# Kernel optimization log

Hardware: AMD Instinct MI355X
Metric: run time of the kernel (lower is better)

## Reference

```python
import jax, jax.numpy as jnp
import numpy as np

B, S, D, H, HD, MLP = 2, 4096, 512, 8, 64, 2048
BLK, C = 128, 32  # Fixed1Pattern(block_size=128), Fixed2Pattern(block_size=128, c=32)
EPS = 1e-6


def _xavier(key, shape, fan_in, fan_out):
    lim = np.sqrt(6.0 / (fan_in + fan_out)).astype(np.float32)
    return jax.random.uniform(key, shape, jnp.float32, -lim, lim)


def setup_inputs() -> dict:
    key = jax.random.key(0)
    ks = jax.random.split(key, 9)
    return {
        "inputs": jax.random.normal(ks[0], (B, S, D), jnp.float32),
        "ln1_scale": jnp.ones((D,), jnp.float32),
        "ln1_bias": jnp.zeros((D,), jnp.float32),
        "wq": _xavier(ks[1], (D, H, HD), D, H * HD),
        "wk": _xavier(ks[2], (D, H, HD), D, H * HD),
        "wv": _xavier(ks[3], (D, H, HD), D, H * HD),
        "wo": _xavier(ks[4], (H, HD, D), H * HD, D),
        "ln2_scale": jnp.ones((D,), jnp.float32),
        "ln2_bias": jnp.zeros((D,), jnp.float32),
        "w1": _xavier(ks[5], (D, MLP), D, MLP),
        "b1": jax.random.normal(ks[6], (MLP,), jnp.float32) * 1e-6,
        "w2": _xavier(ks[7], (MLP, D), MLP, D),
        "b2": jax.random.normal(ks[8], (D,), jnp.float32) * 1e-6,
    }


def _layer_norm(x, scale, bias):
    mu = jnp.mean(x, axis=-1, keepdims=True)
    var = jnp.mean(jnp.square(x - mu), axis=-1, keepdims=True)
    return (x - mu) * jax.lax.rsqrt(var + EPS) * scale + bias


def _sparse_mask():
    # Union of causal Fixed1 (same block) and Fixed2 (last C columns of each block) patterns.
    i = jnp.arange(S)[:, None]
    j = jnp.arange(S)[None, :]
    causal = j <= i
    local = (i // BLK) == (j // BLK)            # Fixed1: within-block
    strided = (j % BLK) >= (BLK - C)            # Fixed2: block-summary columns
    return causal & (local | strided)           # [S, S] bool


def reference(inputs, ln1_scale, ln1_bias, wq, wk, wv, wo,
              ln2_scale, ln2_bias, w1, b1, w2, b2):
    x = _layer_norm(inputs, ln1_scale, ln1_bias)
    q = jnp.einsum("bsd,dhk->bshk", x, wq)
    k = jnp.einsum("bsd,dhk->bshk", x, wk)
    v = jnp.einsum("bsd,dhk->bshk", x, wv)
    scale = 1.0 / np.sqrt(HD).astype(np.float32)
    scores = jnp.einsum("bqhk,bshk->bhqs", q * scale, k)  # [B,H,S,S]
    mask = _sparse_mask()[None, None]
    scores = jnp.where(mask, scores, jnp.float32(-1e9))
    attn = jax.nn.softmax(scores, axis=-1)
    ctx = jnp.einsum("bhqs,bshk->bqhk", attn, v)
    attn_out = jnp.einsum("bqhk,hkd->bqd", ctx, wo)
    x = attn_out + inputs  # residual 1 (dropout deterministic)
    y = _layer_norm(x, ln2_scale, ln2_bias)
    y = jax.nn.gelu(y @ w1 + b1) @ w2 + b2  # MlpBlock
    return x + y
```

## Files before the change

kernel.cpp:

```cpp
#include <hip/hip_runtime.h>
#include <hip/hip_bf16.h>

typedef __attribute__((ext_vector_type(8))) __bf16 bf16x8;
typedef __attribute__((ext_vector_type(8))) short s16x8;
typedef __attribute__((ext_vector_type(4))) float f32x4;

#define NB 2
#define NS 4096
#define ND 512
#define NH 8
#define NHD 64
#define NMLP 2048

__device__ __forceinline__ unsigned short f2b(float f) {
  __hip_bfloat16 h = __float2bfloat16(f);
  return __builtin_bit_cast(unsigned short, h);
}

__device__ __forceinline__ float geluf(float x) {
  float u = 0.7978845608028654f * (x + 0.044715f * x * x * x);
  return x / (1.0f + __expf(-2.0f * u));
}

__device__ __forceinline__ void gload16(const void* g, void* l) {
  __builtin_amdgcn_global_load_lds((const __attribute__((address_space(1))) void*)g,
                                   (__attribute__((address_space(3))) void*)l, 16, 0, 0);
}

__global__ __launch_bounds__(256) void prep_weights(const float* __restrict__ wq,
                                                    const float* __restrict__ wk,
                                                    const float* __restrict__ wv,
                                                    const float* __restrict__ wo,
                                                    const float* __restrict__ w1,
                                                    const float* __restrict__ w2,
                                                    unsigned short* __restrict__ qkvT,
                                                    unsigned short* __restrict__ woT,
                                                    unsigned short* __restrict__ w1T,
                                                    unsigned short* __restrict__ w2T) {
  __shared__ unsigned short lt[64][66];
  const int tile = blockIdx.x, t = threadIdx.x;
  const float* src;
  unsigned short* dst;
  int R, C, tr, tc;
  float sc = 1.0f;
  if (tile < 256) {
    int seg = tile >> 6, tt = tile & 63;
    R = 512; C = 512;
    src = seg == 0 ? wq : seg == 1 ? wk : seg == 2 ? wv : wo;
    dst = (seg < 3) ? (qkvT + ((size_t)seg << 18)) : woT;
    if (seg == 0) sc = 0.125f;
    tr = tt >> 3; tc = tt & 7;
  } else if (tile < 512) {
    int tt = tile - 256;
    R = 512; C = 2048; src = w1; dst = w1T;
    tr = tt >> 5; tc = tt & 31;
  } else {
    int tt = tile - 512;
    R = 2048; C = 512; src = w2; dst = w2T;
    tr = tt >> 3; tc = tt & 7;
  }
  const int r0 = tr * 64, c0 = tc * 64;
  const int fx = t & 15, fy = t >> 4;
#pragma unroll
  for (int p = 0; p < 4; ++p) {
    int rr = p * 16 + fy;
    float4 v = *(const float4*)&src[(size_t)(r0 + rr) * C + c0 + fx * 4];
    lt[rr][fx * 4 + 0] = f2b(v.x * sc);
    lt[rr][fx * 4 + 1] = f2b(v.y * sc);
    lt[rr][fx * 4 + 2] = f2b(v.z * sc);
    lt[rr][fx * 4 + 3] = f2b(v.w * sc);
  }
  __syncthreads();
#pragma unroll
  for (int p = 0; p < 4; ++p) {
    int cc = p * 16 + fy;
    ushort4 o;
    o.x = lt[fx * 4 + 0][cc];
    o.y = lt[fx * 4 + 1][cc];
    o.z = lt[fx * 4 + 2][cc];
    o.w = lt[fx * 4 + 3][cc];
    *(ushort4*)&dst[(size_t)(c0 + cc) * R + r0 + fx * 4] = o;
  }
}

__global__ __launch_bounds__(256) void ln_bf16(const float* __restrict__ x,
                                               const float* __restrict__ g,
                                               const float* __restrict__ bta,
                                               unsigned short* __restrict__ out) {
  const int t = threadIdx.x, l = t & 63, w = t >> 6;
  const size_t row = (size_t)blockIdx.x * 4 + w;
  const float4* xr = (const float4*)(x + row * ND);
  float4 a = xr[l];
  float4 bq = xr[64 + l];
  float s = a.x + a.y + a.z + a.w + bq.x + bq.y + bq.z + bq.w;
  float ss = a.x * a.x + a.y * a.y + a.z * a.z + a.w * a.w +
             bq.x * bq.x + bq.y * bq.y + bq.z * bq.z + bq.w * bq.w;
#pragma unroll
  for (int msk = 1; msk <= 32; msk <<= 1) {
    s += __shfl_xor(s, msk);
    ss += __shfl_xor(ss, msk);
  }
  float mu = s * (1.0f / ND);
  float var = ss * (1.0f / ND) - mu * mu;
  float rr = rsqrtf(var + 1e-6f);
  const float4* g4 = (const float4*)g;
  const float4* b4 = (const float4*)bta;
  float4 g0 = g4[l], g1 = g4[64 + l], b0 = b4[l], b1 = b4[64 + l];
  ushort4 o0, o1;
  o0.x = f2b((a.x - mu) * rr * g0.x + b0.x);
  o0.y = f2b((a.y - mu) * rr * g0.y + b0.y);
  o0.z = f2b((a.z - mu) * rr * g0.z + b0.z);
  o0.w = f2b((a.w - mu) * rr * g0.w + b0.w);
  o1.x = f2b((bq.x - mu) * rr * g1.x + b1.x);
  o1.y = f2b((bq.y - mu) * rr * g1.y + b1.y);
  o1.z = f2b((bq.z - mu) * rr * g1.z + b1.z);
  o1.w = f2b((bq.w - mu) * rr * g1.w + b1.w);
  ushort4* orow = (ushort4*)(out + row * ND);
  orow[l] = o0;
  orow[64 + l] = o1;
}

template <int EPI>
__global__ __launch_bounds__(512, 2) void gemm256(const unsigned short* __restrict__ A,
                                                  const unsigned short* __restrict__ Bt,
                                                  int M, int N, int K,
                                                  unsigned short* __restrict__ ob,
                                                  const float* __restrict__ bias) {
  __shared__ unsigned short lA[2][256 * 64];
  __shared__ unsigned short lB[2][256 * 64];
  const int t = threadIdx.x, l = t & 63, w = t >> 6;
  const int wr = w >> 2, wc = w & 3;
  const int gx = gridDim.x;
  const int nwg = gx * gridDim.y;
  const int fid = blockIdx.y * gx + blockIdx.x;
  const int q8 = nwg >> 3, r8 = nwg & 7, xcd = fid & 7, idx = fid >> 3;
  const int lid = (xcd < r8 ? xcd * (q8 + 1) : r8 * (q8 + 1) + (xcd - r8) * q8) + idx;
  const int bm = lid / gx, bn = lid % gx;
  const size_t rowBytes = (size_t)K * 2;
  const char* Ab = (const char*)A + (size_t)bm * 256 * rowBytes;
  const char* Bb = (const char*)Bt + (size_t)bn * 256 * rowBytes;
  const int srow0 = t >> 3;
  const int scb = (((t & 7) ^ ((t >> 3) & 7)) << 4);
  f32x4 acc[8][4] = {};

  auto stage = [&](int buf, int k0) {
    char* dA = (char*)&lA[buf][0] + t * 16;
    char* dB = (char*)&lB[buf][0] + t * 16;
#pragma unroll
    for (int i = 0; i < 4; ++i) {
      const size_t go = (size_t)(srow0 + i * 64) * rowBytes + 2 * k0 + scb;
      gload16(Ab + go, dA + i * 8192);
      gload16(Bb + go, dB + i * 8192);
    }
  };

  const int nkt = K >> 6;
  stage(0, 0);
  int cur = 0;
  for (int kt = 0; kt < nkt; ++kt) {
    if (kt + 1 < nkt) {
      stage(cur ^ 1, (kt + 1) * 64);
      asm volatile("s_waitcnt vmcnt(8)" ::: "memory");
    } else {
      asm volatile("s_waitcnt vmcnt(0)" ::: "memory");
    }
    __builtin_amdgcn_s_barrier();
    __builtin_amdgcn_sched_barrier(0);
#pragma unroll
    for (int ks = 0; ks < 2; ++ks) {
      const int xg = ((ks * 4 + (l >> 4)) ^ (l & 7)) * 8;
      bf16x8 aF[8], bF[4];
#pragma unroll
      for (int m = 0; m < 8; ++m)
        aF[m] = *(const bf16x8*)&lA[cur][(wr * 128 + m * 16 + (l & 15)) * 64 + xg];
#pragma unroll
      for (int n = 0; n < 4; ++n)
        bF[n] = *(const bf16x8*)&lB[cur][(wc * 64 + n * 16 + (l & 15)) * 64 + xg];
      __builtin_amdgcn_s_setprio(1);
#pragma unroll
      for (int m = 0; m < 8; ++m)
#pragma unroll
        for (int n = 0; n < 4; ++n)
          acc[m][n] = __builtin_amdgcn_mfma_f32_16x16x32_bf16(aF[m], bF[n], acc[m][n], 0, 0, 0);
      __builtin_amdgcn_s_setprio(0);
    }
    asm volatile("s_waitcnt lgkmcnt(0)" ::: "memory");
    __builtin_amdgcn_s_barrier();
    cur ^= 1;
  }
#pragma unroll
  for (int m = 0; m < 8; ++m)
#pragma unroll
    for (int n = 0; n < 4; ++n) {
      int row0 = bm * 256 + wr * 128 + m * 16 + (l >> 4) * 4;
      int col = bn * 256 + wc * 64 + n * 16 + (l & 15);
      if constexpr (EPI == 0) {
        int part = col >> 9, nn = col & 511;
        int hh = nn >> 6, hd = nn & 63;
        int b = row0 >> 12, sidx0 = row0 & 4095;
        if (part < 2) {
#pragma unroll
          for (int j = 0; j < 4; ++j)
            ob[((((size_t)part * NB + b) * NH + hh) * NS + sidx0 + j) * NHD + hd] =
                f2b(acc[m][n][j]);
        } else {
          ushort4 o;
          o.x = f2b(acc[m][n][0]);
          o.y = f2b(acc[m][n][1]);
          o.z = f2b(acc[m][n][2]);
          o.w = f2b(acc[m][n][3]);
          *(ushort4*)&ob[(size_t)2 * NB * NH * NS * NHD +
                         (((size_t)b * NH + hh) * NHD + hd) * NS + sidx0] = o;
        }
      } else {
#pragma unroll
        for (int j = 0; j < 4; ++j) {
          size_t i = (size_t)(row0 + j) * NMLP + col;
          ob[i] = f2b(geluf(acc[m][n][j] + bias[col]));
        }
      }
    }
}

template <int EPI>
__global__ __launch_bounds__(512) void gemm_bt(const unsigned short* __restrict__ A,
                                               const unsigned short* __restrict__ Bt,
                                               int M, int N, int K,
                                               float* __restrict__ of,
                                               const float* __restrict__ addf,
                                               const float* __restrict__ bias) {
  __shared__ unsigned short lA[2][128 * 64];
  __shared__ unsigned short lB[2][128 * 64];
  const int t = threadIdx.x;
  const int l = t & 63, w = t >> 6;
  const int wr = w >> 2, wc = w & 3;
  const int gx = gridDim.x;
  const int nwg = gx * gridDim.y;
  const int fid = blockIdx.y * gx + blockIdx.x;
  const int q8 = nwg >> 3, r8 = nwg & 7, xcd = fid & 7, idx = fid >> 3;
  const int lid = (xcd < r8 ? xcd * (q8 + 1) : r8 * (q8 + 1) + (xcd - r8) * q8) + idx;
  const int bm = lid / gx, bn = lid % gx;
  const size_t rowBytes = (size_t)K * 2;
  const char* Ab = (const char*)A + (size_t)bm * 128 * rowBytes;
  const char* Bb = (const char*)Bt + (size_t)bn * 128 * rowBytes;
  const int sr0 = t >> 3;
  const int scb = (((t & 7) ^ ((t >> 3) & 7)) << 4);
  f32x4 acc[4][2] = {};

  auto stage = [&](int buf, int k0) {
    char* dA = (char*)&lA[buf][0] + t * 16;
    char* dB = (char*)&lB[buf][0] + t * 16;
#pragma unroll
    for (int i = 0; i < 2; ++i) {
      const size_t go = (size_t)(sr0 + i * 64) * rowBytes + 2 * k0 + scb;
      gload16(Ab + go, dA + i * 8192);
      gload16(Bb + go, dB + i * 8192);
    }
  };

  const int nkt = K >> 6;
  stage(0, 0);
  int cur = 0;
  for (int kt = 0; kt < nkt; ++kt) {
    if (kt + 1 < nkt) {
      stage(cur ^ 1, (kt + 1) * 64);
      asm volatile("s_waitcnt vmcnt(4)" ::: "memory");
    } else {
      asm volatile("s_waitcnt vmcnt(0)" ::: "memory");
    }
    __builtin_amdgcn_s_barrier();
    __builtin_amdgcn_sched_barrier(0);
#pragma unroll
    for (int ks = 0; ks < 2; ++ks) {
      const int xg = ((ks * 4 + (l >> 4)) ^ (l & 7)) * 8;
      bf16x8 aF[4], bF[2];
#pragma unroll
      for (int m = 0; m < 4; ++m)
        aF[m] = *(const bf16x8*)&lA[cur][(wr * 64 + m * 16 + (l & 15)) * 64 + xg];
#pragma unroll
      for (int n = 0; n < 2; ++n)
        bF[n] = *(const bf16x8*)&lB[cur][(wc * 32 + n * 16 + (l & 15)) * 64 + xg];
      __builtin_amdgcn_s_setprio(1);
#pragma unroll
      for (int m = 0; m < 4; ++m)
#pragma unroll
        for (int n = 0; n < 2; ++n)
          acc[m][n] = __builtin_amdgcn_mfma_f32_16x16x32_bf16(aF[m], bF[n], acc[m][n], 0, 0, 0);
      __builtin_amdgcn_s_setprio(0);
    }
    asm volatile("s_waitcnt lgkmcnt(0)" ::: "memory");
    __builtin_amdgcn_s_barrier();
    cur ^= 1;
  }
#pragma unroll
  for (int m = 0; m < 4; ++m)
#pragma unroll
    for (int n = 0; n < 2; ++n) {
      int row0 = bm * 128 + wr * 64 + m * 16 + (l >> 4) * 4;
      int col = bn * 128 + wc * 32 + n * 16 + (l & 15);
#pragma unroll
      for (int j = 0; j < 4; ++j) {
        int row = row0 + j;
        float v = acc[m][n][j];
        if constexpr (EPI == 1) {
          size_t i = (size_t)row * ND + col;
          of[i] = v + addf[i];
        } else {
          size_t i = (size_t)row * ND + col;
          of[i] = v + bias[col] + addf[i];
        }
      }
    }
}

__global__ __launch_bounds__(512, 4) void attn_sparse(const unsigned short* __restrict__ qm,
                                                      const unsigned short* __restrict__ km,
                                                      const unsigned short* __restrict__ vTg,
                                                      unsigned short* __restrict__ ctx) {
  __shared__ unsigned short kl[128 * 72];
  __shared__ unsigned short vt[64 * 136];
  __shared__ unsigned short pl[8][16 * 72];
  const int t = threadIdx.x, l = t & 63, w = t >> 6;
  const int bid = blockIdx.x;
  const int hh = bid & 7;
  const int jj = bid >> 3;
  const int b = jj >> 5;
  const int qb = (jj < 32) ? jj : 63 - jj;
  const size_t bh = ((size_t)b * NH + hh) * NS;
  const size_t bhd = ((size_t)b * NH + hh) * NHD;
  const int qrow0 = qb * 128 + w * 16;
  bf16x8 qa[2];
#pragma unroll
  for (int ks = 0; ks < 2; ++ks)
    qa[ks] = *(const bf16x8*)&qm[(bh + qrow0 + (l & 15)) * NHD + ks * 32 + (l >> 4) * 8];
  f32x4 c[4] = {};
  float mrun[4], lrun[4];
#pragma unroll
  for (int j = 0; j < 4; ++j) { mrun[j] = -1e30f; lrun[j] = 0.0f; }

  const int nsum128 = qb >> 2, rem = qb & 3;
  const int nSumCh = nsum128 + (rem ? 1 : 0);
  const int nch = nSumCh + 1;
  const int kkey = t >> 2, kd = (t & 3) * 16;
  const int vd = t >> 3, vk = (t & 7) * 16;

  s16x8 kr0, kr1, vr0, vr1;
  auto issueLoads = [&](int c2) {
    int grK, sV;
    if (c2 < nSumCh) {
      grK = ((c2 << 2) + (kkey >> 5)) * 128 + 96 + (kkey & 31);
      sV = ((c2 << 2) + (vk >> 5)) * 128 + 96 + (vk & 31);
    } else {
      grK = qb * 128 + kkey;
      sV = qb * 128 + vk;
    }
    const unsigned short* kp = &km[(bh + grK) * NHD + kd];
    kr0 = *(const s16x8*)kp;
    kr1 = *(const s16x8*)(kp + 8);
    const unsigned short* vp = &vTg[(bhd + vd) * NS + sV];
    vr0 = *(const s16x8*)vp;
    vr1 = *(const s16x8*)(vp + 8);
  };

  issueLoads(0);
  for (int ch = 0; ch < nch; ++ch) {
    if (ch) {
      asm volatile("s_waitcnt lgkmcnt(0)" ::: "memory");
      __builtin_amdgcn_s_barrier();
    }
    *(s16x8*)&kl[kkey * 72 + kd] = kr0;
    *(s16x8*)&kl[kkey * 72 + kd + 8] = kr1;
    *(s16x8*)&vt[vd * 136 + vk] = vr0;
    *(s16x8*)&vt[vd * 136 + vk + 8] = vr1;
    asm volatile("s_waitcnt lgkmcnt(0)" ::: "memory");
    __builtin_amdgcn_s_barrier();
    __builtin_amdgcn_sched_barrier(0);
    if (ch + 1 < nch) issueLoads(ch + 1);

    const bool isLocal = (ch == nch - 1);
    const bool isRem = (rem != 0) && !isLocal && (ch == nsum128);
    const int nT = isLocal ? (w + 1) : (isRem ? 2 * rem : 8);
    const int nTpl = isLocal ? ((w | 1) + 1) : nT;
    const int nKs = nTpl >> 1;

    f32x4 sf[8];
#pragma unroll
    for (int n = 0; n < 8; ++n) {
      if (n < nT) {
        const bf16x8 k0 = *(const bf16x8*)&kl[(n * 16 + (l & 15)) * 72 + (l >> 4) * 8];
        const bf16x8 k1 = *(const bf16x8*)&kl[(n * 16 + (l & 15)) * 72 + 32 + (l >> 4) * 8];
        f32x4 a = {};
        a = __builtin_amdgcn_mfma_f32_16x16x32_bf16(qa[0], k0, a, 0, 0, 0);
        a = __builtin_amdgcn_mfma_f32_16x16x32_bf16(qa[1], k1, a, 0, 0, 0);
        if (isLocal && n == w) {
#pragma unroll
          for (int j = 0; j < 4; ++j)
            if ((l & 15) > (l >> 4) * 4 + j) a[j] = -1e9f;
        }
        sf[n] = a;
      }
    }
    float cm[4];
#pragma unroll
    for (int j = 0; j < 4; ++j) cm[j] = -1e30f;
#pragma unroll
    for (int n = 0; n < 8; ++n)
      if (n < nT)
#pragma unroll
        for (int j = 0; j < 4; ++j) cm[j] = fmaxf(cm[j], sf[n][j]);
#pragma unroll
    for (int j = 0; j < 4; ++j) {
      cm[j] = fmaxf(cm[j], __shfl_xor(cm[j], 1));
      cm[j] = fmaxf(cm[j], __shfl_xor(cm[j], 2));
      cm[j] = fmaxf(cm[j], __shfl_xor(cm[j], 4));
      cm[j] = fmaxf(cm[j], __shfl_xor(cm[j], 8));
    }
    bool need = false;
#pragma unroll
    for (int j = 0; j < 4; ++j) need |= (cm[j] > mrun[j] + 8.0f);
    if (__any(need)) {
      float al[4];
#pragma unroll
      for (int j = 0; j < 4; ++j) {
        float nm = fmaxf(mrun[j], cm[j]);
        al[j] = __expf(mrun[j] - nm);
        mrun[j] = nm;
      }
#pragma unroll
      for (int n = 0; n < 4; ++n)
#pragma unroll
        for (int j = 0; j < 4; ++j) c[n][j] *= al[j];
#pragma unroll
      for (int j = 0; j < 4; ++j) lrun[j] *= al[j];
    }
    float rs[4] = {0.f, 0.f, 0.f, 0.f};
#pragma unroll
    for (int n = 0; n < 8; ++n)
      if (n < nT)
#pragma unroll
        for (int j = 0; j < 4; ++j) {
          float p = __expf(sf[n][j] - mrun[j]);
          sf[n][j] = p;
          rs[j] += p;
        }
#pragma unroll
    for (int j = 0; j < 4; ++j) {
      rs[j] += __shfl_xor(rs[j], 1);
      rs[j] += __shfl_xor(rs[j], 2);
      rs[j] += __shfl_xor(rs[j], 4);
      rs[j] += __shfl_xor(rs[j], 8);
      lrun[j] += rs[j];
    }
#pragma unroll
    for (int h = 0; h < 2; ++h) {
      if (h * 4 < nTpl) {
#pragma unroll
        for (int n2 = 0; n2 < 4; ++n2) {
          const int n = h * 4 + n2;
#pragma unroll
          for (int j = 0; j < 4; ++j) {
            if (n < nTpl) {
              unsigned short pv = 0;
              if (n < nT) pv = f2b(sf[n][j]);
              pl[w][((l >> 4) * 4 + j) * 72 + n2 * 16 + (l & 15)] = pv;
            }
          }
        }
#pragma unroll
        for (int ks2 = 0; ks2 < 2; ++ks2) {
          const int ks = h * 2 + ks2;
          if (ks < nKs) {
            const bf16x8 pa = *(const bf16x8*)&pl[w][(l & 15) * 72 + ks2 * 32 + (l >> 4) * 8];
#pragma unroll
            for (int nd = 0; nd < 4; ++nd) {
              const bf16x8 vb =
                  *(const bf16x8*)&vt[(nd * 16 + (l & 15)) * 136 + ks * 32 + (l >> 4) * 8];
              c[nd] = __builtin_amdgcn_mfma_f32_16x16x32_bf16(pa, vb, c[nd], 0, 0, 0);
            }
          }
        }
      }
    }
  }
  float rinv[4];
#pragma unroll
  for (int j = 0; j < 4; ++j) rinv[j] = 1.0f / lrun[j];
#pragma unroll
  for (int n = 0; n < 4; ++n)
#pragma unroll
    for (int j = 0; j < 4; ++j) {
      int srow = qrow0 + (l >> 4) * 4 + j;
      int col = n * 16 + (l & 15);
      ctx[((size_t)b * NS + srow) * ND + hh * NHD + col] = f2b(c[n][j] * rinv[j]);
    }
}

extern "C" void kernel_launch(void* const* d_in, const int* in_sizes, int n_in,
                              void* d_out, int out_size, void* d_ws, size_t ws_size,
                              hipStream_t stream) {
  (void)in_sizes; (void)n_in; (void)out_size; (void)ws_size;
  const float* inputs = (const float*)d_in[0];
  const float* ln1s = (const float*)d_in[1];
  const float* ln1b = (const float*)d_in[2];
  const float* wq = (const float*)d_in[3];
  const float* wk = (const float*)d_in[4];
  const float* wv = (const float*)d_in[5];
  const float* wo = (const float*)d_in[6];
  const float* ln2s = (const float*)d_in[7];
  const float* ln2b = (const float*)d_in[8];
  const float* w1 = (const float*)d_in[9];
  const float* b1 = (const float*)d_in[10];
  const float* w2 = (const float*)d_in[11];
  const float* b2 = (const float*)d_in[12];
  float* out = (float*)d_out;

  unsigned short* xln = (unsigned short*)d_ws;
  unsigned short* xln2 = xln + (size_t)8192 * 512;
  unsigned short* ctx = xln2 + (size_t)8192 * 512;
  unsigned short* qkv = ctx + (size_t)8192 * 512;
  float* xres = (float*)(qkv + (size_t)3 * 8192 * 512);
  unsigned short* hbuf = (unsigned short*)(xres + (size_t)8192 * 512);
  unsigned short* qkvT = hbuf + (size_t)8192 * 2048;
  unsigned short* woT = qkvT + (size_t)1536 * 512;
  unsigned short* w1T = woT + (size_t)512 * 512;
  unsigned short* w2T = w1T + (size_t)2048 * 512;

  prep_weights<<<768, 256, 0, stream>>>(wq, wk, wv, wo, w1, w2, qkvT, woT, w1T, w2T);
  ln_bf16<<<2048, 256, 0, stream>>>(inputs, ln1s, ln1b, xln);
  gemm256<0><<<dim3(6, 32), 512, 0, stream>>>(xln, qkvT, 8192, 1536, 512, qkv, nullptr);
  attn_sparse<<<512, 512, 0, stream>>>(qkv, qkv + (size_t)8192 * 512,
                                       qkv + (size_t)2 * 8192 * 512, ctx);
  gemm_bt<1><<<dim3(4, 64), 512, 0, stream>>>(ctx, woT, 8192, 512, 512,
                                              xres, inputs, nullptr);
  ln_bf16<<<2048, 256, 0, stream>>>(xres, ln2s, ln2b, xln2);
  gemm256<2><<<dim3(8, 32), 512, 0, stream>>>(xln2, w1T, 8192, 2048, 512, hbuf, b1);
  gemm_bt<3><<<dim3(4, 64), 512, 0, stream>>>(hbuf, w2T, 8192, 512, 2048,
                                              out, xres, b2);
}
```

Baseline: 161.5 us.

## Drop 256-tile GEMM, swizzle attention LDS, use exp2 softmax with prescaled Q

Removes the 256x256 gemm256 kernel and routes the QKV and MLP-up GEMMs through the 128x128 gemm_bt kernel with the same epilogues, giving more workgroups. The attention kernel replaces padded LDS layouts for K, V and P with XOR-swizzled unpadded layouts, and wraps its MFMAs in setprio. Softmax now uses raw v_exp_f32 (exp2), with log2(e) folded into the Q weight scale and the rescale threshold adjusted to match. Smaller GEMM tiles lower data reuse per tile, and the exp2 path changes the numerics slightly.

```diff
diff --git a/kernel.cpp b/kernel.cpp
--- a/kernel.cpp
+++ b/kernel.cpp
@@ -20,6 +20,12 @@
 __device__ __forceinline__ float geluf(float x) {
   float u = 0.7978845608028654f * (x + 0.044715f * x * x * x);
   return x / (1.0f + __expf(-2.0f * u));
+}
+
+__device__ __forceinline__ float exp2_fast(float x) {
+  float r;
+  asm("v_exp_f32 %0, %1" : "=v"(r) : "v"(x));
+  return r;
 }
 
 __device__ __forceinline__ void gload16(const void* g, void* l) {
@@ -48,7 +54,7 @@
     R = 512; C = 512;
     src = seg == 0 ? wq : seg == 1 ? wk : seg == 2 ? wv : wo;
     dst = (seg < 3) ? (qkvT + ((size_t)seg << 18)) : woT;
-    if (seg == 0) sc = 0.125f;
+    if (seg == 0) sc = 0.18033688011112042f;
     tr = tt >> 3; tc = tt & 7;
   } else if (tile < 512) {
     int tt = tile - 256;
@@ -121,111 +127,10 @@
 }
 
 template <int EPI>
-__global__ __launch_bounds__(512, 2) void gemm256(const unsigned short* __restrict__ A,
-                                                  const unsigned short* __restrict__ Bt,
-                                                  int M, int N, int K,
-                                                  unsigned short* __restrict__ ob,
-                                                  const float* __restrict__ bias) {
-  __shared__ unsigned short lA[2][256 * 64];
-  __shared__ unsigned short lB[2][256 * 64];
-  const int t = threadIdx.x, l = t & 63, w = t >> 6;
-  const int wr = w >> 2, wc = w & 3;
-  const int gx = gridDim.x;
-  const int nwg = gx * gridDim.y;
-  const int fid = blockIdx.y * gx + blockIdx.x;
-  const int q8 = nwg >> 3, r8 = nwg & 7, xcd = fid & 7, idx = fid >> 3;
-  const int lid = (xcd < r8 ? xcd * (q8 + 1) : r8 * (q8 + 1) + (xcd - r8) * q8) + idx;
-  const int bm = lid / gx, bn = lid % gx;
-  const size_t rowBytes = (size_t)K * 2;
-  const char* Ab = (const char*)A + (size_t)bm * 256 * rowBytes;
-  const char* Bb = (const char*)Bt + (size_t)bn * 256 * rowBytes;
-  const int srow0 = t >> 3;
-  const int scb = (((t & 7) ^ ((t >> 3) & 7)) << 4);
-  f32x4 acc[8][4] = {};
-
-  auto stage = [&](int buf, int k0) {
-    char* dA = (char*)&lA[buf][0] + t * 16;
-    char* dB = (char*)&lB[buf][0] + t * 16;
-#pragma unroll
-    for (int i = 0; i < 4; ++i) {
-      const size_t go = (size_t)(srow0 + i * 64) * rowBytes + 2 * k0 + scb;
-      gload16(Ab + go, dA + i * 8192);
-      gload16(Bb + go, dB + i * 8192);
-    }
-  };
-
-  const int nkt = K >> 6;
-  stage(0, 0);
-  int cur = 0;
-  for (int kt = 0; kt < nkt; ++kt) {
-    if (kt + 1 < nkt) {
-      stage(cur ^ 1, (kt + 1) * 64);
-      asm volatile("s_waitcnt vmcnt(8)" ::: "memory");
-    } else {
-      asm volatile("s_waitcnt vmcnt(0)" ::: "memory");
-    }
-    __builtin_amdgcn_s_barrier();
-    __builtin_amdgcn_sched_barrier(0);
-#pragma unroll
-    for (int ks = 0; ks < 2; ++ks) {
-      const int xg = ((ks * 4 + (l >> 4)) ^ (l & 7)) * 8;
-      bf16x8 aF[8], bF[4];
-#pragma unroll
-      for (int m = 0; m < 8; ++m)
-        aF[m] = *(const bf16x8*)&lA[cur][(wr * 128 + m * 16 + (l & 15)) * 64 + xg];
-#pragma unroll
-      for (int n = 0; n < 4; ++n)
-        bF[n] = *(const bf16x8*)&lB[cur][(wc * 64 + n * 16 + (l & 15)) * 64 + xg];
-      __builtin_amdgcn_s_setprio(1);
-#pragma unroll
-      for (int m = 0; m < 8; ++m)
-#pragma unroll
-        for (int n = 0; n < 4; ++n)
-          acc[m][n] = __builtin_amdgcn_mfma_f32_16x16x32_bf16(aF[m], bF[n], acc[m][n], 0, 0, 0);
-      __builtin_amdgcn_s_setprio(0);
-    }
-    asm volatile("s_waitcnt lgkmcnt(0)" ::: "memory");
-    __builtin_amdgcn_s_barrier();
-    cur ^= 1;
-  }
-#pragma unroll
-  for (int m = 0; m < 8; ++m)
-#pragma unroll
-    for (int n = 0; n < 4; ++n) {
-      int row0 = bm * 256 + wr * 128 + m * 16 + (l >> 4) * 4;
-      int col = bn * 256 + wc * 64 + n * 16 + (l & 15);
-      if constexpr (EPI == 0) {
-        int part = col >> 9, nn = col & 511;
-        int hh = nn >> 6, hd = nn & 63;
-        int b = row0 >> 12, sidx0 = row0 & 4095;
-        if (part < 2) {
-#pragma unroll
-          for (int j = 0; j < 4; ++j)
-            ob[((((size_t)part * NB + b) * NH + hh) * NS + sidx0 + j) * NHD + hd] =
-                f2b(acc[m][n][j]);
-        } else {
-          ushort4 o;
-          o.x = f2b(acc[m][n][0]);
-          o.y = f2b(acc[m][n][1]);
-          o.z = f2b(acc[m][n][2]);
-          o.w = f2b(acc[m][n][3]);
-          *(ushort4*)&ob[(size_t)2 * NB * NH * NS * NHD +
-                         (((size_t)b * NH + hh) * NHD + hd) * NS + sidx0] = o;
-        }
-      } else {
-#pragma unroll
-        for (int j = 0; j < 4; ++j) {
-          size_t i = (size_t)(row0 + j) * NMLP + col;
-          ob[i] = f2b(geluf(acc[m][n][j] + bias[col]));
-        }
-      }
-    }
-}
-
-template <int EPI>
 __global__ __launch_bounds__(512) void gemm_bt(const unsigned short* __restrict__ A,
                                                const unsigned short* __restrict__ Bt,
                                                int M, int N, int K,
+                                               unsigned short* __restrict__ ob,
                                                float* __restrict__ of,
                                                const float* __restrict__ addf,
                                                const float* __restrict__ bias) {
@@ -298,16 +203,42 @@
     for (int n = 0; n < 2; ++n) {
       int row0 = bm * 128 + wr * 64 + m * 16 + (l >> 4) * 4;
       int col = bn * 128 + wc * 32 + n * 16 + (l & 15);
-#pragma unroll
-      for (int j = 0; j < 4; ++j) {
-        int row = row0 + j;
-        float v = acc[m][n][j];
-        if constexpr (EPI == 1) {
-          size_t i = (size_t)row * ND + col;
-          of[i] = v + addf[i];
+      if constexpr (EPI == 0) {
+        int part = col >> 9, nn = col & 511;
+        int hh = nn >> 6, hd = nn & 63;
+        int b = row0 >> 12, sidx0 = row0 & 4095;
+        if (part < 2) {
+#pragma unroll
+          for (int j = 0; j < 4; ++j)
+            ob[((((size_t)part * NB + b) * NH + hh) * NS + sidx0 + j) * NHD + hd] =
+                f2b(acc[m][n][j]);
         } else {
-          size_t i = (size_t)row * ND + col;
-          of[i] = v + bias[col] + addf[i];
+          ushort4 o;
+          o.x = f2b(acc[m][n][0]);
+          o.y = f2b(acc[m][n][1]);
+          o.z = f2b(acc[m][n][2]);
+          o.w = f2b(acc[m][n][3]);
+          *(ushort4*)&ob[(size_t)2 * NB * NH * NS * NHD +
+                         (((size_t)b * NH + hh) * NHD + hd) * NS + sidx0] = o;
+        }
+      } else if constexpr (EPI == 2) {
+#pragma unroll
+        for (int j = 0; j < 4; ++j) {
+          size_t i = (size_t)(row0 + j) * NMLP + col;
+          ob[i] = f2b(geluf(acc[m][n][j] + bias[col]));
+        }
+      } else {
+#pragma unroll
+        for (int j = 0; j < 4; ++j) {
+          int row = row0 + j;
+          float v = acc[m][n][j];
+          if constexpr (EPI == 1) {
+            size_t i = (size_t)row * ND + col;
+            of[i] = v + addf[i];
+          } else {
+            size_t i = (size_t)row * ND + col;
+            of[i] = v + bias[col] + addf[i];
+          }
         }
       }
     }
@@ -317,9 +248,9 @@
                                                       const unsigned short* __restrict__ km,
                                                       const unsigned short* __restrict__ vTg,
                                                       unsigned short* __restrict__ ctx) {
-  __shared__ unsigned short kl[128 * 72];
-  __shared__ unsigned short vt[64 * 136];
-  __shared__ unsigned short pl[8][16 * 72];
+  __shared__ unsigned short kl[128 * 64];
+  __shared__ unsigned short vt[64 * 128];
+  __shared__ unsigned short pl[8][16 * 64];
   const int t = threadIdx.x, l = t & 63, w = t >> 6;
   const int bid = blockIdx.x;
   const int hh = bid & 7;
@@ -341,25 +272,24 @@
   const int nsum128 = qb >> 2, rem = qb & 3;
   const int nSumCh = nsum128 + (rem ? 1 : 0);
   const int nch = nSumCh + 1;
-  const int kkey = t >> 2, kd = (t & 3) * 16;
-  const int vd = t >> 3, vk = (t & 7) * 16;
-
-  s16x8 kr0, kr1, vr0, vr1;
+  const int sr = t >> 3, sg = t & 7;
+
+  s16x8 kr[2], vr[2];
   auto issueLoads = [&](int c2) {
-    int grK, sV;
-    if (c2 < nSumCh) {
-      grK = ((c2 << 2) + (kkey >> 5)) * 128 + 96 + (kkey & 31);
-      sV = ((c2 << 2) + (vk >> 5)) * 128 + 96 + (vk & 31);
-    } else {
-      grK = qb * 128 + kkey;
-      sV = qb * 128 + vk;
-    }
-    const unsigned short* kp = &km[(bh + grK) * NHD + kd];
-    kr0 = *(const s16x8*)kp;
-    kr1 = *(const s16x8*)(kp + 8);
-    const unsigned short* vp = &vTg[(bhd + vd) * NS + sV];
-    vr0 = *(const s16x8*)vp;
-    vr1 = *(const s16x8*)(vp + 8);
+#pragma unroll
+    for (int i = 0; i < 2; ++i) {
+      const int r = sr + 64 * i;
+      const int grK = (c2 < nSumCh) ? ((c2 * 4 + (r >> 5)) * 128 + 96 + (r & 31))
+                                    : (qb * 128 + r);
+      kr[i] = *(const s16x8*)&km[(bh + grK) * NHD + sg * 8];
+    }
+#pragma unroll
+    for (int i = 0; i < 2; ++i) {
+      const int cc = sg * 8 + 64 * i;
+      const int gk = (c2 < nSumCh) ? ((c2 * 4 + (cc >> 5)) * 128 + 96 + (cc & 31))
+                                   : (qb * 128 + cc);
+      vr[i] = *(const s16x8*)&vTg[(bhd + sr) * NS + gk];
+    }
   };
 
   issueLoads(0);
@@ -368,10 +298,14 @@
       asm volatile("s_waitcnt lgkmcnt(0)" ::: "memory");
       __builtin_amdgcn_s_barrier();
     }
-    *(s16x8*)&kl[kkey * 72 + kd] = kr0;
-    *(s16x8*)&kl[kkey * 72 + kd + 8] = kr1;
-    *(s16x8*)&vt[vd * 136 + vk] = vr0;
-    *(s16x8*)&vt[vd * 136 + vk + 8] = vr1;
+#pragma unroll
+    for (int i = 0; i < 2; ++i) {
+      const int r = sr + 64 * i;
+      *(s16x8*)&kl[r * 64 + ((sg ^ (r & 7)) << 3)] = kr[i];
+    }
+#pragma unroll
+    for (int i = 0; i < 2; ++i)
+      *(s16x8*)&vt[sr * 128 + 64 * i + ((sg ^ (sr & 7)) << 3)] = vr[i];
     asm volatile("s_waitcnt lgkmcnt(0)" ::: "memory");
     __builtin_amdgcn_s_barrier();
     __builtin_amdgcn_sched_barrier(0);
@@ -387,11 +321,14 @@
 #pragma unroll
     for (int n = 0; n < 8; ++n) {
       if (n < nT) {
-        const bf16x8 k0 = *(const bf16x8*)&kl[(n * 16 + (l & 15)) * 72 + (l >> 4) * 8];
-        const bf16x8 k1 = *(const bf16x8*)&kl[(n * 16 + (l & 15)) * 72 + 32 + (l >> 4) * 8];
+        const int row = n * 16 + (l & 15);
+        const bf16x8 k0 = *(const bf16x8*)&kl[row * 64 + (((l >> 4) ^ (l & 7)) << 3)];
+        const bf16x8 k1 = *(const bf16x8*)&kl[row * 64 + (((4 + (l >> 4)) ^ (l & 7)) << 3)];
         f32x4 a = {};
+        __builtin_amdgcn_s_setprio(1);
         a = __builtin_amdgcn_mfma_f32_16x16x32_bf16(qa[0], k0, a, 0, 0, 0);
         a = __builtin_amdgcn_mfma_f32_16x16x32_bf16(qa[1], k1, a, 0, 0, 0);
+        __builtin_amdgcn_s_setprio(0);
         if (isLocal && n == w) {
 #pragma unroll
           for (int j = 0; j < 4; ++j)
@@ -417,13 +354,13 @@
     }
     bool need = false;
 #pragma unroll
-    for (int j = 0; j < 4; ++j) need |= (cm[j] > mrun[j] + 8.0f);
+    for (int j = 0; j < 4; ++j) need |= (cm[j] > mrun[j] + 11.54f);
     if (__any(need)) {
       float al[4];
 #pragma unroll
       for (int j = 0; j < 4; ++j) {
         float nm = fmaxf(mrun[j], cm[j]);
-        al[j] = __expf(mrun[j] - nm);
+        al[j] = exp2_fast(mrun[j] - nm);
         mrun[j] = nm;
       }
 #pragma unroll
@@ -439,7 +376,7 @@
       if (n < nT)
 #pragma unroll
         for (int j = 0; j < 4; ++j) {
-          float p = __expf(sf[n][j] - mrun[j]);
+          float p = exp2_fast(sf[n][j] - mrun[j]);
           sf[n][j] = p;
           rs[j] += p;
         }
@@ -462,7 +399,9 @@
             if (n < nTpl) {
               unsigned short pv = 0;
               if (n < nT) pv = f2b(sf[n][j]);
-              pl[w][((l >> 4) * 4 + j) * 72 + n2 * 16 + (l & 15)] = pv;
+              const int rowp = (l >> 4) * 4 + j;
+              const int up = (n2 * 2 + ((l & 15) >> 3)) ^ (rowp & 7);
+              pl[w][rowp * 64 + up * 8 + (l & 7)] = pv;
             }
           }
         }
@@ -470,13 +409,17 @@
         for (int ks2 = 0; ks2 < 2; ++ks2) {
           const int ks = h * 2 + ks2;
           if (ks < nKs) {
-            const bf16x8 pa = *(const bf16x8*)&pl[w][(l & 15) * 72 + ks2 * 32 + (l >> 4) * 8];
+            const bf16x8 pa =
+                *(const bf16x8*)&pl[w][(l & 15) * 64 + (((ks2 * 4 + (l >> 4)) ^ (l & 7)) << 3)];
+            __builtin_amdgcn_s_setprio(1);
 #pragma unroll
             for (int nd = 0; nd < 4; ++nd) {
-              const bf16x8 vb =
-                  *(const bf16x8*)&vt[(nd * 16 + (l & 15)) * 136 + ks * 32 + (l >> 4) * 8];
+              const int u = ks * 4 + (l >> 4);
+              const bf16x8 vb = *(const bf16x8*)&vt[(nd * 16 + (l & 15)) * 128 +
+                                                    (((u & 8) | ((u & 7) ^ (l & 7))) << 3)];
               c[nd] = __builtin_amdgcn_mfma_f32_16x16x32_bf16(pa, vb, c[nd], 0, 0, 0);
             }
+            __builtin_amdgcn_s_setprio(0);
           }
         }
       }
@@ -527,13 +470,15 @@
 
   prep_weights<<<768, 256, 0, stream>>>(wq, wk, wv, wo, w1, w2, qkvT, woT, w1T, w2T);
   ln_bf16<<<2048, 256, 0, stream>>>(inputs, ln1s, ln1b, xln);
-  gemm256<0><<<dim3(6, 32), 512, 0, stream>>>(xln, qkvT, 8192, 1536, 512, qkv, nullptr);
+  gemm_bt<0><<<dim3(12, 64), 512, 0, stream>>>(xln, qkvT, 8192, 1536, 512,
+                                               qkv, nullptr, nullptr, nullptr);
   attn_sparse<<<512, 512, 0, stream>>>(qkv, qkv + (size_t)8192 * 512,
                                        qkv + (size_t)2 * 8192 * 512, ctx);
   gemm_bt<1><<<dim3(4, 64), 512, 0, stream>>>(ctx, woT, 8192, 512, 512,
-                                              xres, inputs, nullptr);
+                                              nullptr, xres, inputs, nullptr);
   ln_bf16<<<2048, 256, 0, stream>>>(xres, ln2s, ln2b, xln2);
-  gemm256<2><<<dim3(8, 32), 512, 0, stream>>>(xln2, w1T, 8192, 2048, 512, hbuf, b1);
+  gemm_bt<2><<<dim3(16, 64), 512, 0, stream>>>(xln2, w1T, 8192, 2048, 512,
+                                               hbuf, nullptr, nullptr, b1);
   gemm_bt<3><<<dim3(4, 64), 512, 0, stream>>>(hbuf, w2T, 8192, 512, 2048,
-                                              out, xres, b2);
-}
+                                              nullptr, out, xres, b2);
+}
```

After: 177.6 us. +10.0%, slower.
